# Kernel optimization log

Measured on AMD Instinct MI355X. Metric: run time of the kernel, lower is better.

The kernel has to match this reference:

```python
import jax, jax.numpy as jnp
import numpy as np

VOCAB, EMBED, MAXLEN, UNITS, F1, BATCH = 50000, 256, 512, 32, 16, 512

def setup_inputs() -> dict:
    key = jax.random.key(0)
    ks = jax.random.split(key, 9)
    tokens = jax.random.randint(ks[0], (BATCH, MAXLEN), 0, VOCAB, dtype=jnp.int32)
    emb_table = jax.random.normal(ks[1], (VOCAB, EMBED), dtype=jnp.float32) * 0.02
    # SimpleRNN params (Keras: kernel, recurrent_kernel, bias)
    Wx = jax.random.normal(ks[2], (EMBED, UNITS), dtype=jnp.float32) * (1.0 / np.sqrt(EMBED))
    Wh = jax.random.normal(ks[3], (UNITS, UNITS), dtype=jnp.float32) * (1.0 / np.sqrt(UNITS))
    b  = jnp.zeros((UNITS,), dtype=jnp.float32)
    W1 = jax.random.normal(ks[4], (UNITS, F1), dtype=jnp.float32) * (1.0 / np.sqrt(UNITS))
    b1 = jnp.zeros((F1,), dtype=jnp.float32)
    W2 = jax.random.normal(ks[5], (F1, 1), dtype=jnp.float32) * (1.0 / np.sqrt(F1))
    b2 = jnp.zeros((1,), dtype=jnp.float32)
    return {"tokens": tokens, "emb_table": emb_table, "Wx": Wx, "Wh": Wh, "b": b,
            "W1": W1, "b1": b1, "W2": W2, "b2": b2}

def reference(tokens, emb_table, Wx, Wh, b, W1, b1, W2, b2):
    # Embedding lookup: [B, T, E]
    x = emb_table[tokens]
    # SimpleRNN recurrence (tanh), return last hidden state. Dropout disabled (inference).
    xs = jnp.transpose(x, (1, 0, 2))  # time-major [T, B, E]
    h0 = jnp.zeros((tokens.shape[0], Wh.shape[0]), dtype=x.dtype)

    def step(h, x_t):
        h_new = jnp.tanh(x_t @ Wx + h @ Wh + b)
        return h_new, None

    h_last, _ = jax.lax.scan(step, h0, xs)
    # Flatten is a no-op on [B, 32]; Dense heads are linear (no activation), then sigmoid.
    z = (h_last @ W1 + b1) @ W2 + b2
    return jax.nn.sigmoid(z)  # [B, 1]
```

## Files before the change

### kernel.cpp

```cpp
#include <hip/hip_runtime.h>
#include <hip/hip_bf16.h>
#include <math.h>

#define TT 512
#define BB 512
#define EE 256
#define UU 32
#define FF1 16

__device__ __forceinline__ void fma4(float4& a, float s, const float4& v) {
    a.x = fmaf(s, v.x, a.x); a.y = fmaf(s, v.y, a.y);
    a.z = fmaf(s, v.z, a.z); a.w = fmaf(s, v.w, a.w);
}

__device__ __forceinline__ float fast_tanh(float x) {
    float e = __builtin_amdgcn_exp2f(x * 2.8853900817779268f);
    float r = __builtin_amdgcn_rcpf(e + 1.0f);
    return fmaf(-2.0f, r, 1.0f);
}

__device__ __forceinline__ float rdlane(float v, int lane) {
    return __int_as_float(__builtin_amdgcn_readlane(__float_as_int(v), lane));
}

__global__ __launch_bounds__(64) void proj_gemv(
    const float* __restrict__ emb, const float* __restrict__ Wx,
    const float* __restrict__ bias, float* __restrict__ P, int nrows)
{
    const int lane = threadIdx.x;
    const int ug = lane & 7;
    const int rg = lane >> 3;
    const int r0 = blockIdx.x * 32 + rg * 4;

    const float4* xp[4];
    #pragma unroll
    for (int i = 0; i < 4; ++i) {
        int r = r0 + i; if (r > nrows - 1) r = nrows - 1;
        xp[i] = (const float4*)(emb + (size_t)r * EE);
    }
    const float4* wxp = (const float4*)Wx + ug;

    float4 acc[4];
    #pragma unroll
    for (int i = 0; i < 4; ++i) acc[i] = make_float4(0.f, 0.f, 0.f, 0.f);

    float4 xqA[4], xqB[4], wqA[4], wqB[4];
    #pragma unroll
    for (int i = 0; i < 4; ++i) xqA[i] = xp[i][0];
    #pragma unroll
    for (int kk = 0; kk < 4; ++kk) wqA[kk] = wxp[kk * 8];

    for (int k4 = 0; k4 < 64; k4 += 2) {
        #pragma unroll
        for (int i = 0; i < 4; ++i) xqB[i] = xp[i][k4 + 1];
        #pragma unroll
        for (int kk = 0; kk < 4; ++kk) wqB[kk] = wxp[(4 * (k4 + 1) + kk) * 8];
        #pragma unroll
        for (int i = 0; i < 4; ++i) {
            fma4(acc[i], xqA[i].x, wqA[0]);
            fma4(acc[i], xqA[i].y, wqA[1]);
            fma4(acc[i], xqA[i].z, wqA[2]);
            fma4(acc[i], xqA[i].w, wqA[3]);
        }
        const int kn = (k4 + 2) & 63;
        #pragma unroll
        for (int i = 0; i < 4; ++i) xqA[i] = xp[i][kn];
        #pragma unroll
        for (int kk = 0; kk < 4; ++kk) wqA[kk] = wxp[(4 * kn + kk) * 8];
        #pragma unroll
        for (int i = 0; i < 4; ++i) {
            fma4(acc[i], xqB[i].x, wqB[0]);
            fma4(acc[i], xqB[i].y, wqB[1]);
            fma4(acc[i], xqB[i].z, wqB[2]);
            fma4(acc[i], xqB[i].w, wqB[3]);
        }
    }

    const float4 bq = ((const float4*)bias)[ug];
    #pragma unroll
    for (int i = 0; i < 4; ++i) {
        const int r = r0 + i;
        if (r < nrows) {
            float4 o = acc[i];
            o.x += bq.x; o.y += bq.y; o.z += bq.z; o.w += bq.w;
            *((float4*)(P + (size_t)r * UU) + ug) = o;
        }
    }
}

__global__ __launch_bounds__(64) void scan_heads(
    const int* __restrict__ tokens, const float* __restrict__ P,
    const float* __restrict__ Wh,
    const float* __restrict__ W1, const float* __restrict__ b1,
    const float* __restrict__ W2, const float* __restrict__ b2,
    float* __restrict__ out)
{
    __shared__ float xs[TT * UU];

    const int L = threadIdx.x;
    const int u = L & 31;
    const int b = blockIdx.x;
    const int* trow = tokens + b * TT;

    float wh[UU];
    #pragma unroll
    for (int k = 0; k < UU; ++k) wh[k] = Wh[k * UU + u];

    const int sub = L >> 3;
    const int q   = L & 7;
    for (int c = 0; c < 8; ++c) {
        int tk8[8];
        #pragma unroll
        for (int i = 0; i < 8; ++i)
            tk8[i] = trow[c * 64 + i * 8 + sub];
        #pragma unroll
        for (int i = 0; i < 8; ++i) {
            const float* src = P + (size_t)tk8[i] * UU + q * 4;
            float* dst = xs + (c * 64 + i * 8) * UU;
            __builtin_amdgcn_global_load_lds(
                (const __attribute__((address_space(1))) void*)src,
                (__attribute__((address_space(3))) void*)dst, 16, 0, 0);
        }
    }
    __syncthreads();

    float xr[4];
    #pragma unroll
    for (int j = 0; j < 4; ++j) xr[j] = xs[j * UU + u];

    float h = 0.f;

    for (int t = 0; t < TT; t += 4) {
        #pragma unroll
        for (int j = 0; j < 4; ++j) {
            float xn = xs[((t + 4 + j) & (TT - 1)) * UU + u];

            float a0 = xr[j], a1 = 0.f, a2 = 0.f, a3 = 0.f;
            #pragma unroll
            for (int k = 0; k < UU; k += 4) {
                float h0 = rdlane(h, k);
                float h1 = rdlane(h, k + 1);
                float h2 = rdlane(h, k + 2);
                float h3 = rdlane(h, k + 3);
                a0 = fmaf(h0, wh[k],     a0);
                a1 = fmaf(h1, wh[k + 1], a1);
                a2 = fmaf(h2, wh[k + 2], a2);
                a3 = fmaf(h3, wh[k + 3], a3);
            }
            h = fast_tanh((a0 + a1) + (a2 + a3));
            xr[j] = xn;
        }
    }

    const int j = threadIdx.x & 15;
    float s = b1[j];
    #pragma unroll
    for (int k = 0; k < UU; ++k) {
        float hk = rdlane(h, k);
        s = fmaf(hk, W1[k * FF1 + j], s);
    }
    float z = b2[0];
    #pragma unroll
    for (int jj = 0; jj < FF1; ++jj) {
        float yj = rdlane(s, jj);
        z = fmaf(yj, W2[jj], z);
    }
    if (threadIdx.x == 0) {
        float e = __builtin_amdgcn_exp2f(-z * 1.4426950408889634f);
        out[b] = __builtin_amdgcn_rcpf(1.0f + e);
    }
}

extern "C" void kernel_launch(void* const* d_in, const int* in_sizes, int n_in,
                              void* d_out, int out_size, void* d_ws, size_t ws_size,
                              hipStream_t stream) {
    const int*   tokens = (const int*)  d_in[0];
    const float* emb    = (const float*)d_in[1];
    const float* Wx     = (const float*)d_in[2];
    const float* Wh     = (const float*)d_in[3];
    const float* bias   = (const float*)d_in[4];
    const float* W1     = (const float*)d_in[5];
    const float* b1     = (const float*)d_in[6];
    const float* W2     = (const float*)d_in[7];
    const float* b2     = (const float*)d_in[8];
    float* out = (float*)d_out;

    const int vocab = in_sizes[1] / EE;
    float* P = (float*)d_ws;

    proj_gemv<<<dim3((vocab + 31) / 32), dim3(64), 0, stream>>>(
        emb, Wx, bias, P, vocab);

    scan_heads<<<dim3(BB), dim3(64), 0, stream>>>(
        tokens, P, Wh, W1, b1, W2, b2, out);
}
```

Measured before the change: 192.5 us.

## Split recurrent matvec across wave halves with bpermute; shrink projection rows per block

The scan kernel now splits the 32-wide recurrent dot product across the two 32-lane halves of the wavefront. Each half computes 16 terms, fetching hidden values via ds_bpermute instead of scalar readlane, and the partial sums are combined with a cross-half bpermute. This is meant to halve the serial per-step chain, at the cost of LDS-permute latency on the critical path. The projection kernel now handles 2 rows per lane group instead of 4, which doubles the grid, and drops the bounds clamps by assuming vocab is divisible by 16.

```diff
diff --git a/kernel.cpp b/kernel.cpp
--- a/kernel.cpp
+++ b/kernel.cpp
@@ -23,6 +23,11 @@
     return __int_as_float(__builtin_amdgcn_readlane(__float_as_int(v), lane));
 }
 
+__device__ __forceinline__ float bperm(int addr_bytes, float v) {
+    return __int_as_float(
+        __builtin_amdgcn_ds_bpermute(addr_bytes, __float_as_int(v)));
+}
+
 __global__ __launch_bounds__(64) void proj_gemv(
     const float* __restrict__ emb, const float* __restrict__ Wx,
     const float* __restrict__ bias, float* __restrict__ P, int nrows)
@@ -30,62 +35,43 @@
     const int lane = threadIdx.x;
     const int ug = lane & 7;
     const int rg = lane >> 3;
-    const int r0 = blockIdx.x * 32 + rg * 4;
+    const int r0 = blockIdx.x * 16 + rg * 2;
 
-    const float4* xp[4];
-    #pragma unroll
-    for (int i = 0; i < 4; ++i) {
-        int r = r0 + i; if (r > nrows - 1) r = nrows - 1;
-        xp[i] = (const float4*)(emb + (size_t)r * EE);
-    }
+    const float4* xp0 = (const float4*)(emb + (size_t)r0 * EE);
+    const float4* xp1 = (const float4*)(emb + (size_t)(r0 + 1) * EE);
     const float4* wxp = (const float4*)Wx + ug;
 
-    float4 acc[4];
+    float4 acc0 = make_float4(0.f, 0.f, 0.f, 0.f);
+    float4 acc1 = make_float4(0.f, 0.f, 0.f, 0.f);
+
+    float4 xA0, xA1, xB0, xB1, wA[4], wB[4];
+    xA0 = xp0[0]; xA1 = xp1[0];
     #pragma unroll
-    for (int i = 0; i < 4; ++i) acc[i] = make_float4(0.f, 0.f, 0.f, 0.f);
-
-    float4 xqA[4], xqB[4], wqA[4], wqB[4];
-    #pragma unroll
-    for (int i = 0; i < 4; ++i) xqA[i] = xp[i][0];
-    #pragma unroll
-    for (int kk = 0; kk < 4; ++kk) wqA[kk] = wxp[kk * 8];
+    for (int kk = 0; kk < 4; ++kk) wA[kk] = wxp[kk * 8];
 
     for (int k4 = 0; k4 < 64; k4 += 2) {
+        xB0 = xp0[k4 + 1]; xB1 = xp1[k4 + 1];
         #pragma unroll
-        for (int i = 0; i < 4; ++i) xqB[i] = xp[i][k4 + 1];
+        for (int kk = 0; kk < 4; ++kk) wB[kk] = wxp[(4 * (k4 + 1) + kk) * 8];
+        fma4(acc0, xA0.x, wA[0]); fma4(acc0, xA0.y, wA[1]);
+        fma4(acc0, xA0.z, wA[2]); fma4(acc0, xA0.w, wA[3]);
+        fma4(acc1, xA1.x, wA[0]); fma4(acc1, xA1.y, wA[1]);
+        fma4(acc1, xA1.z, wA[2]); fma4(acc1, xA1.w, wA[3]);
+        const int kn = (k4 + 2) & 63;
+        xA0 = xp0[kn]; xA1 = xp1[kn];
         #pragma unroll
-        for (int kk = 0; kk < 4; ++kk) wqB[kk] = wxp[(4 * (k4 + 1) + kk) * 8];
-        #pragma unroll
-        for (int i = 0; i < 4; ++i) {
-            fma4(acc[i], xqA[i].x, wqA[0]);
-            fma4(acc[i], xqA[i].y, wqA[1]);
-            fma4(acc[i], xqA[i].z, wqA[2]);
-            fma4(acc[i], xqA[i].w, wqA[3]);
-        }
-        const int kn = (k4 + 2) & 63;
-        #pragma unroll
-        for (int i = 0; i < 4; ++i) xqA[i] = xp[i][kn];
-        #pragma unroll
-        for (int kk = 0; kk < 4; ++kk) wqA[kk] = wxp[(4 * kn + kk) * 8];
-        #pragma unroll
-        for (int i = 0; i < 4; ++i) {
-            fma4(acc[i], xqB[i].x, wqB[0]);
-            fma4(acc[i], xqB[i].y, wqB[1]);
-            fma4(acc[i], xqB[i].z, wqB[2]);
-            fma4(acc[i], xqB[i].w, wqB[3]);
-        }
+        for (int kk = 0; kk < 4; ++kk) wA[kk] = wxp[(4 * kn + kk) * 8];
+        fma4(acc0, xB0.x, wB[0]); fma4(acc0, xB0.y, wB[1]);
+        fma4(acc0, xB0.z, wB[2]); fma4(acc0, xB0.w, wB[3]);
+        fma4(acc1, xB1.x, wB[0]); fma4(acc1, xB1.y, wB[1]);
+        fma4(acc1, xB1.z, wB[2]); fma4(acc1, xB1.w, wB[3]);
     }
 
     const float4 bq = ((const float4*)bias)[ug];
-    #pragma unroll
-    for (int i = 0; i < 4; ++i) {
-        const int r = r0 + i;
-        if (r < nrows) {
-            float4 o = acc[i];
-            o.x += bq.x; o.y += bq.y; o.z += bq.z; o.w += bq.w;
-            *((float4*)(P + (size_t)r * UU) + ug) = o;
-        }
-    }
+    acc0.x += bq.x; acc0.y += bq.y; acc0.z += bq.z; acc0.w += bq.w;
+    acc1.x += bq.x; acc1.y += bq.y; acc1.z += bq.z; acc1.w += bq.w;
+    *((float4*)(P + (size_t)r0 * UU) + ug)       = acc0;
+    *((float4*)(P + (size_t)(r0 + 1) * UU) + ug) = acc1;
 }
 
 __global__ __launch_bounds__(64) void scan_heads(
@@ -99,12 +85,16 @@
 
     const int L = threadIdx.x;
     const int u = L & 31;
+    const int hi = L >> 5;
     const int b = blockIdx.x;
     const int* trow = tokens + b * TT;
 
-    float wh[UU];
+    float wh[16];
     #pragma unroll
-    for (int k = 0; k < UU; ++k) wh[k] = Wh[k * UU + u];
+    for (int j = 0; j < 16; ++j) wh[j] = Wh[(hi * 16 + j) * UU + u];
+
+    const int pbase = hi * 64;
+    const int xaddr = (L ^ 32) * 4;
 
     const int sub = L >> 3;
     const int q   = L & 7;
@@ -135,29 +125,31 @@
         for (int j = 0; j < 4; ++j) {
             float xn = xs[((t + 4 + j) & (TT - 1)) * UU + u];
 
-            float a0 = xr[j], a1 = 0.f, a2 = 0.f, a3 = 0.f;
+            float p0 = 0.f, p1 = 0.f, p2 = 0.f, p3 = 0.f;
             #pragma unroll
-            for (int k = 0; k < UU; k += 4) {
-                float h0 = rdlane(h, k);
-                float h1 = rdlane(h, k + 1);
-                float h2 = rdlane(h, k + 2);
-                float h3 = rdlane(h, k + 3);
-                a0 = fmaf(h0, wh[k],     a0);
-                a1 = fmaf(h1, wh[k + 1], a1);
-                a2 = fmaf(h2, wh[k + 2], a2);
-                a3 = fmaf(h3, wh[k + 3], a3);
+            for (int k = 0; k < 16; k += 4) {
+                float h0 = bperm(pbase + (k + 0) * 4, h);
+                float h1 = bperm(pbase + (k + 1) * 4, h);
+                float h2 = bperm(pbase + (k + 2) * 4, h);
+                float h3 = bperm(pbase + (k + 3) * 4, h);
+                p0 = fmaf(h0, wh[k],     p0);
+                p1 = fmaf(h1, wh[k + 1], p1);
+                p2 = fmaf(h2, wh[k + 2], p2);
+                p3 = fmaf(h3, wh[k + 3], p3);
             }
-            h = fast_tanh((a0 + a1) + (a2 + a3));
+            float ps = (p0 + p1) + (p2 + p3);
+            float other = bperm(xaddr, ps);
+            h = fast_tanh((ps + other) + xr[j]);
             xr[j] = xn;
         }
     }
 
-    const int j = threadIdx.x & 15;
-    float s = b1[j];
+    const int jh = L & 15;
+    float s = b1[jh];
     #pragma unroll
     for (int k = 0; k < UU; ++k) {
         float hk = rdlane(h, k);
-        s = fmaf(hk, W1[k * FF1 + j], s);
+        s = fmaf(hk, W1[k * FF1 + jh], s);
     }
     float z = b2[0];
     #pragma unroll
@@ -165,7 +157,7 @@
         float yj = rdlane(s, jj);
         z = fmaf(yj, W2[jj], z);
     }
-    if (threadIdx.x == 0) {
+    if (L == 0) {
         float e = __builtin_amdgcn_exp2f(-z * 1.4426950408889634f);
         out[b] = __builtin_amdgcn_rcpf(1.0f + e);
     }
@@ -188,7 +180,7 @@
     const int vocab = in_sizes[1] / EE;
     float* P = (float*)d_ws;
 
-    proj_gemv<<<dim3((vocab + 31) / 32), dim3(64), 0, stream>>>(
+    proj_gemv<<<dim3(vocab / 16), dim3(64), 0, stream>>>(
         emb, Wx, bias, P, vocab);
 
     scan_heads<<<dim3(BB), dim3(64), 0, stream>>>(
```

New measurement: 216.5 us. +12.5%, slower.

## Remap vocab projection to one row per thread with uniform Wx loads

Applied to the files above, without the earlier changes.

Rewrites the vocabulary projection kernel so each thread computes a full 32-wide output row, with the Wx weights read at wave-uniform addresses (likely scalar loads) instead of per-lane vector loads. This is meant to cut redundant Wx vector-memory traffic and the per-lane weight registers. In exchange each lane reads its own 1 KB embedding row with strided float4 accesses, which coalesce poorly across the wave. The grid is halved to 64 rows per block.

```diff
diff --git a/kernel.cpp b/kernel.cpp
--- a/kernel.cpp
+++ b/kernel.cpp
@@ -7,11 +7,6 @@
 #define EE 256
 #define UU 32
 #define FF1 16
-
-__device__ __forceinline__ void fma4(float4& a, float s, const float4& v) {
-    a.x = fmaf(s, v.x, a.x); a.y = fmaf(s, v.y, a.y);
-    a.z = fmaf(s, v.z, a.z); a.w = fmaf(s, v.w, a.w);
-}
 
 __device__ __forceinline__ float fast_tanh(float x) {
     float e = __builtin_amdgcn_exp2f(x * 2.8853900817779268f);
@@ -23,68 +18,55 @@
     return __int_as_float(__builtin_amdgcn_readlane(__float_as_int(v), lane));
 }
 
-__global__ __launch_bounds__(64) void proj_gemv(
+__global__ __launch_bounds__(64) void proj_rows(
     const float* __restrict__ emb, const float* __restrict__ Wx,
     const float* __restrict__ bias, float* __restrict__ P, int nrows)
 {
-    const int lane = threadIdx.x;
-    const int ug = lane & 7;
-    const int rg = lane >> 3;
-    const int r0 = blockIdx.x * 32 + rg * 4;
+    int r = blockIdx.x * 64 + threadIdx.x;
+    if (r >= nrows) r = nrows - 1;
+    const float4* xp = (const float4*)(emb + (size_t)r * EE);
 
-    const float4* xp[4];
+    float acc[UU];
     #pragma unroll
-    for (int i = 0; i < 4; ++i) {
-        int r = r0 + i; if (r > nrows - 1) r = nrows - 1;
-        xp[i] = (const float4*)(emb + (size_t)r * EE);
-    }
-    const float4* wxp = (const float4*)Wx + ug;
+    for (int u = 0; u < UU; ++u) acc[u] = 0.f;
 
-    float4 acc[4];
-    #pragma unroll
-    for (int i = 0; i < 4; ++i) acc[i] = make_float4(0.f, 0.f, 0.f, 0.f);
-
-    float4 xqA[4], xqB[4], wqA[4], wqB[4];
-    #pragma unroll
-    for (int i = 0; i < 4; ++i) xqA[i] = xp[i][0];
-    #pragma unroll
-    for (int kk = 0; kk < 4; ++kk) wqA[kk] = wxp[kk * 8];
-
-    for (int k4 = 0; k4 < 64; k4 += 2) {
-        #pragma unroll
-        for (int i = 0; i < 4; ++i) xqB[i] = xp[i][k4 + 1];
-        #pragma unroll
-        for (int kk = 0; kk < 4; ++kk) wqB[kk] = wxp[(4 * (k4 + 1) + kk) * 8];
+    auto stage = [&](const float4* xq, int kbase) {
         #pragma unroll
         for (int i = 0; i < 4; ++i) {
-            fma4(acc[i], xqA[i].x, wqA[0]);
-            fma4(acc[i], xqA[i].y, wqA[1]);
-            fma4(acc[i], xqA[i].z, wqA[2]);
-            fma4(acc[i], xqA[i].w, wqA[3]);
+            const float xc[4] = {xq[i].x, xq[i].y, xq[i].z, xq[i].w};
+            #pragma unroll
+            for (int c = 0; c < 4; ++c) {
+                const float* w = Wx + (size_t)(kbase + i * 4 + c) * UU;
+                #pragma unroll
+                for (int u = 0; u < UU; ++u)
+                    acc[u] = fmaf(xc[c], w[u], acc[u]);
+            }
         }
-        const int kn = (k4 + 2) & 63;
+    };
+
+    float4 xA[4], xB[4];
+    #pragma unroll
+    for (int i = 0; i < 4; ++i) xA[i] = xp[i];
+
+    #pragma unroll 1
+    for (int m = 0; m < 16; m += 2) {
         #pragma unroll
-        for (int i = 0; i < 4; ++i) xqA[i] = xp[i][kn];
+        for (int i = 0; i < 4; ++i) xB[i] = xp[(m + 1) * 4 + i];
+        stage(xA, m * 16);
         #pragma unroll
-        for (int kk = 0; kk < 4; ++kk) wqA[kk] = wxp[(4 * kn + kk) * 8];
-        #pragma unroll
-        for (int i = 0; i < 4; ++i) {
-            fma4(acc[i], xqB[i].x, wqB[0]);
-            fma4(acc[i], xqB[i].y, wqB[1]);
-            fma4(acc[i], xqB[i].z, wqB[2]);
-            fma4(acc[i], xqB[i].w, wqB[3]);
-        }
+        for (int i = 0; i < 4; ++i) xA[i] = xp[((m + 2) & 15) * 4 + i];
+        stage(xB, (m + 1) * 16);
     }
 
-    const float4 bq = ((const float4*)bias)[ug];
+    float4* o = (float4*)(P + (size_t)r * UU);
     #pragma unroll
-    for (int i = 0; i < 4; ++i) {
-        const int r = r0 + i;
-        if (r < nrows) {
-            float4 o = acc[i];
-            o.x += bq.x; o.y += bq.y; o.z += bq.z; o.w += bq.w;
-            *((float4*)(P + (size_t)r * UU) + ug) = o;
-        }
+    for (int j4 = 0; j4 < 8; ++j4) {
+        float4 v;
+        v.x = acc[j4 * 4 + 0] + bias[j4 * 4 + 0];
+        v.y = acc[j4 * 4 + 1] + bias[j4 * 4 + 1];
+        v.z = acc[j4 * 4 + 2] + bias[j4 * 4 + 2];
+        v.w = acc[j4 * 4 + 3] + bias[j4 * 4 + 3];
+        o[j4] = v;
     }
 }
 
@@ -188,7 +170,7 @@
     const int vocab = in_sizes[1] / EE;
     float* P = (float*)d_ws;
 
-    proj_gemv<<<dim3((vocab + 31) / 32), dim3(64), 0, stream>>>(
+    proj_rows<<<dim3((vocab + 63) / 64), dim3(64), 0, stream>>>(
         emb, Wx, bias, P, vocab);
 
     scan_heads<<<dim3(BB), dim3(64), 0, stream>>>(
```

Measured after the change: 217.4 us. 1.13x slower.
